# Kernel tuning notes

Hardware: AMD Instinct MI355X
Metric: run time of the kernel (lower is better)

The kernel has to match this reference:

```python
import jax, jax.numpy as jnp
import numpy as np

M, IN, OUT, K = 16384, 1024, 1024, 12


def setup_inputs() -> dict:
    key = jax.random.key(0)
    ks = jax.random.split(key, 7)
    x = jax.random.normal(ks[0], (M, IN), dtype=jnp.float32)
    # grid: per-feature linspace(-2,2) plus noise so the per-row sort is nontrivial
    base = jnp.linspace(-2.0, 2.0, K, dtype=jnp.float32)
    grid = jnp.broadcast_to(base, (IN, K)) + 0.3 * jax.random.normal(ks[1], (IN, K), dtype=jnp.float32)
    coeffs = 0.1 * jax.random.normal(ks[2], (IN, K), dtype=jnp.float32)
    knot_alive = 3.0 * jnp.ones((IN, K), dtype=jnp.float32) + 0.5 * jax.random.normal(ks[3], (IN, K), dtype=jnp.float32)
    proj_w = jax.random.normal(ks[4], (OUT, IN), dtype=jnp.float32) / np.sqrt(IN)
    proj_b = jax.random.normal(ks[5], (OUT,), dtype=jnp.float32) * 0.01
    res_w = jax.random.normal(ks[6], (OUT, IN), dtype=jnp.float32) / np.sqrt(IN)
    return {"x": x, "grid": grid, "coeffs": coeffs, "knot_alive": knot_alive,
            "proj_w": proj_w, "proj_b": proj_b, "res_w": res_w}


def _eval_adaptive_spline(x, grid, coeffs, knot_alive):
    # x: (M, in)  grid/coeffs/knot_alive: (in, K)
    K_ = grid.shape[1]
    sort_idx = jnp.argsort(grid, axis=1)
    sorted_grid = jnp.take_along_axis(grid, sort_idx, axis=1)
    sorted_coeffs = jnp.take_along_axis(coeffs, sort_idx, axis=1)
    sorted_alive = jnp.take_along_axis(knot_alive, sort_idx, axis=1)
    masked_coeffs = sorted_coeffs * jax.nn.sigmoid(sorted_alive)  # (in, K)

    grid_min = sorted_grid[:, 0]   # (in,)
    grid_max = sorted_grid[:, -1]  # (in,)
    x_clamped = jnp.minimum(jnp.maximum(x, grid_min[None, :]), grid_max[None, :])
    grid_range = jnp.maximum(grid_max - grid_min, 1e-6)
    x_norm = (x_clamped - grid_min[None, :]) / grid_range[None, :] * (K_ - 1)  # (M, in)
    idx_l = jnp.clip(x_norm.astype(jnp.int32), 0, K_ - 2)  # trunc == floor (x_norm >= 0)
    frac = x_norm - idx_l.astype(x.dtype)

    feat = jnp.arange(x.shape[1])[None, :]  # (1, in)
    c_left = masked_coeffs[feat, idx_l]      # (M, in)
    c_right = masked_coeffs[feat, idx_l + 1]  # (M, in)
    return c_left + frac * (c_right - c_left)


def reference(x, grid, coeffs, knot_alive, proj_w, proj_b, res_w):
    spline_out = _eval_adaptive_spline(x, grid, coeffs, knot_alive)  # (M, in)
    return spline_out @ proj_w.T + proj_b + x @ res_w.T  # (M, out)
```

## Files before the change

kernel.cpp:

```cpp
#include <hip/hip_runtime.h>
#include <hip/hip_bf16.h>

typedef unsigned short u16;
typedef float f32x4 __attribute__((ext_vector_type(4)));
typedef __bf16 bf16x8 __attribute__((ext_vector_type(8)));
typedef u16 u16x8 __attribute__((ext_vector_type(8)));

#define M_DIM 16384
#define IN_DIM 1024
#define OUT_DIM 1024
#define K_KNOTS 12
#define KCAT 2048


__device__ __forceinline__ u16 f2bf(float f) {
    unsigned int u = __builtin_bit_cast(unsigned int, f);
    u = u + 0x7FFFu + ((u >> 16) & 1u);
    return (u16)(u >> 16);
}

__device__ __forceinline__ void gload_lds16(const void* g, void* l) {
    __builtin_amdgcn_global_load_lds(
        (const __attribute__((address_space(1))) unsigned int*)g,
        (__attribute__((address_space(3))) unsigned int*)l, 16, 0, 0);
}

__global__ void prep_kernel(const float* __restrict__ grid,
                            const float* __restrict__ coeffs,
                            const float* __restrict__ alive,
                            float* __restrict__ pmc,
                            float* __restrict__ pgmin,
                            float* __restrict__ pscale)
{
    int i = blockIdx.x * blockDim.x + threadIdx.x;
    if (i >= IN_DIM) return;
    float g[K_KNOTS], c[K_KNOTS], a[K_KNOTS];
    for (int k = 0; k < K_KNOTS; ++k) {
        g[k] = grid[i * K_KNOTS + k];
        c[k] = coeffs[i * K_KNOTS + k];
        a[k] = alive[i * K_KNOTS + k];
    }
    for (int k = 1; k < K_KNOTS; ++k) {
        float gk = g[k], ck = c[k], ak = a[k];
        int j = k - 1;
        while (j >= 0 && g[j] > gk) {
            g[j + 1] = g[j]; c[j + 1] = c[j]; a[j + 1] = a[j]; --j;
        }
        g[j + 1] = gk; c[j + 1] = ck; a[j + 1] = ak;
    }
    for (int k = 0; k < K_KNOTS; ++k)
        pmc[i * K_KNOTS + k] = c[k] / (1.0f + expf(-a[k]));
    pgmin[i] = g[0];
    pscale[i] = (float)(K_KNOTS - 1) / fmaxf(g[K_KNOTS - 1] - g[0], 1e-6f);
}

__global__ __launch_bounds__(256) void conv_w_kernel(
    const float* __restrict__ pw, const float* __restrict__ rw,
    u16* __restrict__ Bw)
{
    const int n16 = blockIdx.x;
    const int tid = threadIdx.x;
    #pragma unroll 1
    for (int j = 0; j < 16; ++j) {
        int s = j * 256 + tid;
        int kc = s >> 6, l = s & 63;
        int row = n16 * 16 + (l & 15);
        int k = kc * 32 + ((l >> 4) & 3) * 8;
        const float* src = (k < IN_DIM) ? &pw[(long)row * IN_DIM + k]
                                        : &rw[(long)row * IN_DIM + (k - IN_DIM)];
        float4 v0 = *(const float4*)src;
        float4 v1 = *(const float4*)(src + 4);
        u16x8 ov;
        ov[0] = f2bf(v0.x); ov[1] = f2bf(v0.y); ov[2] = f2bf(v0.z); ov[3] = f2bf(v0.w);
        ov[4] = f2bf(v1.x); ov[5] = f2bf(v1.y); ov[6] = f2bf(v1.z); ov[7] = f2bf(v1.w);
        *(u16x8*)&Bw[((long)n16 * 64 + kc) * 512 + l * 8] = ov;
    }
}

#define XT_STR 260

__global__ __launch_bounds__(256) void build_a_kernel(
    const float* __restrict__ x,
    const float* __restrict__ pmc,
    const float* __restrict__ pgmin,
    const float* __restrict__ pscale,
    u16* __restrict__ Abf)
{
    __shared__ float s_mc[IN_DIM * K_KNOTS];
    __shared__ float s_gmin[IN_DIM];
    __shared__ float s_scale[IN_DIM];
    __shared__ float xt[16 * XT_STR];
    const int tid = threadIdx.x;
    for (int i = tid; i < IN_DIM * K_KNOTS; i += 256) s_mc[i] = pmc[i];
    for (int i = tid; i < IN_DIM; i += 256) { s_gmin[i] = pgmin[i]; s_scale[i] = pscale[i]; }

    const int m16 = blockIdx.x;

    #pragma unroll 1
    for (int c0 = 0; c0 < IN_DIM; c0 += 256) {
        __syncthreads();

        #pragma unroll
        for (int p = 0; p < 4; ++p) {
            int idx = p * 256 + tid;
            int r = idx >> 6, lc = (idx & 63) * 4;
            float4 v = *(const float4*)&x[(long)(m16 * 16 + r) * IN_DIM + c0 + lc];
            *(float4*)&xt[r * XT_STR + lc] = v;
        }
        __syncthreads();

        #pragma unroll
        for (int p = 0; p < 2; ++p) {
            int s = p * 256 + tid;
            int kc_l = s >> 6, l = s & 63;
            int r = l & 15;
            int cb = kc_l * 32 + ((l >> 4) & 3) * 8;
            const float* xp = &xt[r * XT_STR + cb];
            float4 v0 = *(const float4*)xp;
            float4 v1 = *(const float4*)(xp + 4);
            float xs[8] = {v0.x, v0.y, v0.z, v0.w, v1.x, v1.y, v1.z, v1.w};
            u16x8 so, co;
            #pragma unroll
            for (int e = 0; e < 8; ++e) {
                int i = c0 + cb + e;
                float xx = xs[e];
                float xn = (xx - s_gmin[i]) * s_scale[i];
                xn = fminf(fmaxf(xn, 0.0f), (float)(K_KNOTS - 1));
                int li = (int)xn;
                if (li > K_KNOTS - 2) li = K_KNOTS - 2;
                float frac = xn - (float)li;
                float cl = s_mc[i * K_KNOTS + li];
                float cr = s_mc[i * K_KNOTS + li + 1];
                so[e] = f2bf(cl + frac * (cr - cl));
                co[e] = f2bf(xx);
            }
            long kcS = (long)m16 * 64 + (c0 >> 5) + kc_l;
            *(u16x8*)&Abf[kcS * 512 + l * 8] = so;
            *(u16x8*)&Abf[(kcS + 32) * 512 + l * 8] = co;
        }
    }
}

#define TBK 64
#define NT (KCAT / TBK)
#define MSTR 32768L

#define BAR()     asm volatile("s_barrier" ::: "memory")
#define VM6BAR()  asm volatile("s_waitcnt vmcnt(6)\ns_barrier" ::: "memory")
#define LGKM0()   do { asm volatile("s_waitcnt lgkmcnt(0)" ::: "memory"); \
                       __builtin_amdgcn_sched_barrier(0); } while (0)

#define READ_A(buf, kk, mh) \
    _Pragma("unroll") \
    for (int m_ = 0; m_ < 4; ++m_) \
        af[m_] = *(const bf16x8*)&lds[(buf) + (kk)*8192 + (wm*8 + (mh)*4 + m_)*512 + loff];

#define READ_B(buf, kk) \
    _Pragma("unroll") \
    for (int n_ = 0; n_ < 4; ++n_) \
        bfr[n_] = *(const bf16x8*)&lds[32768 + (buf) + (kk)*8192 + (wn*4 + n_)*512 + loff];

#define MFMA16(base) \
    __builtin_amdgcn_s_setprio(1); \
    _Pragma("unroll") \
    for (int m_ = 0; m_ < 4; ++m_) \
        _Pragma("unroll") \
        for (int n_ = 0; n_ < 4; ++n_) \
            acc[(base) + m_][n_] = __builtin_amdgcn_mfma_f32_16x16x32_bf16( \
                af[m_], bfr[n_], acc[(base) + m_][n_], 0, 0, 0); \
    __builtin_amdgcn_s_setprio(0);

#define STAGE_A(Tidx, kk, buf) do { \
    gload_lds16(pAf +          ((long)((Tidx)*2 + (kk))) * 512, &lds[(buf) + (kk)*8192 + d0]); \
    gload_lds16(pAf + 8*MSTR + ((long)((Tidx)*2 + (kk))) * 512, &lds[(buf) + (kk)*8192 + d1]); } while (0)
#define STAGE_B(Tidx, kk, buf) do { \
    gload_lds16(pBf +          ((long)((Tidx)*2 + (kk))) * 512, &lds[32768 + (buf) + (kk)*8192 + d0]); \
    gload_lds16(pBf + 8*MSTR + ((long)((Tidx)*2 + (kk))) * 512, &lds[32768 + (buf) + (kk)*8192 + d1]); } while (0)

__global__ __launch_bounds__(512, 2) void gemm_kernel(
    const u16* __restrict__ A,
    const u16* __restrict__ B,
    const float* __restrict__ bias,
    float* __restrict__ C)
{
    __shared__ __align__(16) u16 lds[65536];

    const int tid  = threadIdx.x;
    const int lane = tid & 63;
    const int wave = tid >> 6;
    const int wm   = wave >> 2;
    const int wn   = wave & 3;

    int wgid = (blockIdx.x & 7) * 32 + (blockIdx.x >> 3);
    const int brow = (wgid >> 2) * 256;
    const int bcol = (wgid & 3) * 256;

    const u16* pAf = A + ((long)(brow >> 4) + wave) * MSTR + lane * 8;
    const u16* pBf = B + ((long)(bcol >> 4) + wave) * MSTR + lane * 8;

    const int d0 = tid * 8;
    const int d1 = 4096 + tid * 8;
    const int loff = lane * 8;

    f32x4 acc[8][4] = {};
    bf16x8 af[4], bfr[4];

    STAGE_A(0, 0, 0);
    STAGE_B(0, 0, 0);
    STAGE_A(0, 1, 0);
    STAGE_B(0, 1, 0);
    STAGE_B(1, 0, 16384);
    STAGE_A(1, 0, 16384);
    STAGE_B(1, 1, 16384);
    VM6BAR();

    #pragma unroll 1
    for (int t = 0; t < NT / 2; ++t) {
        const int T  = 2 * t;
        const int T1 = T + 1;
        const int T2 = (T + 2 < NT) ? T + 2 : 0;
        const int T3 = (T + 3 < NT) ? T + 3 : 0;

        READ_A(0, 0, 0); READ_B(0, 0);
        STAGE_A(T1, 1, 16384);
        BAR(); LGKM0();
        MFMA16(0);
        BAR();

        READ_A(0, 0, 1);
        STAGE_B(T2, 0, 0);
        BAR(); LGKM0();
        MFMA16(4);
        BAR();

        READ_A(0, 1, 0); READ_B(0, 1);
        STAGE_A(T2, 0, 0);
        BAR(); LGKM0();
        MFMA16(0);
        BAR();

        READ_A(0, 1, 1);
        STAGE_B(T2, 1, 0);
        VM6BAR(); LGKM0();
        MFMA16(4);
        BAR();

        READ_A(16384, 0, 0); READ_B(16384, 0);
        STAGE_A(T2, 1, 0);
        BAR(); LGKM0();
        MFMA16(0);
        BAR();

        READ_A(16384, 0, 1);
        STAGE_B(T3, 0, 16384);
        BAR(); LGKM0();
        MFMA16(4);
        BAR();

        READ_A(16384, 1, 0); READ_B(16384, 1);
        STAGE_A(T3, 0, 16384);
        BAR(); LGKM0();
        MFMA16(0);
        BAR();

        READ_A(16384, 1, 1);
        STAGE_B(T3, 1, 16384);
        VM6BAR(); LGKM0();
        MFMA16(4);
        BAR();
    }

    const int crow0 = brow + wm * 128 + (lane >> 4) * 4;
    const int ccol0 = bcol + wn * 64 + (lane & 15);
    float bv[4];
    #pragma unroll
    for (int n = 0; n < 4; ++n) bv[n] = bias[ccol0 + n * 16];
    #pragma unroll
    for (int m = 0; m < 8; ++m) {
        #pragma unroll
        for (int n = 0; n < 4; ++n) {
            #pragma unroll
            for (int j = 0; j < 4; ++j) {
                int row = crow0 + m * 16 + j;
                C[(long)row * OUT_DIM + ccol0 + n * 16] = acc[m][n][j] + bv[n];
            }
        }
    }
}

extern "C" void kernel_launch(void* const* d_in, const int* in_sizes, int n_in,
                              void* d_out, int out_size, void* d_ws, size_t ws_size,
                              hipStream_t stream) {
    const float* x      = (const float*)d_in[0];
    const float* grid   = (const float*)d_in[1];
    const float* coeffs = (const float*)d_in[2];
    const float* alive  = (const float*)d_in[3];
    const float* proj_w = (const float*)d_in[4];
    const float* proj_b = (const float*)d_in[5];
    const float* res_w  = (const float*)d_in[6];
    float* out = (float*)d_out;

    char* w = (char*)d_ws;
    size_t a_bytes = (size_t)M_DIM * KCAT * sizeof(u16);
    size_t b_bytes = (size_t)OUT_DIM * KCAT * sizeof(u16);
    u16* Abf   = (u16*)w;
    u16* Bw    = (u16*)(w + a_bytes);
    float* pmc = (float*)(w + a_bytes + b_bytes);
    float* pgmin  = pmc + IN_DIM * K_KNOTS;
    float* pscale = pgmin + IN_DIM;

    prep_kernel<<<(IN_DIM + 255) / 256, 256, 0, stream>>>(grid, coeffs, alive,
                                                          pmc, pgmin, pscale);
    conv_w_kernel<<<OUT_DIM / 16, 256, 0, stream>>>(proj_w, res_w, Bw);
    build_a_kernel<<<M_DIM / 16, 256, 0, stream>>>(x, pmc, pgmin, pscale, Abf);
    gemm_kernel<<<(M_DIM / 256) * (OUT_DIM / 256), 512, 0, stream>>>(Abf, Bw, proj_b, out);
}
```

Measured before the change: 114.7 us.

## Shrink GEMM tile to 128x256 with simple double buffer; batch spline rows

The GEMM kernel drops from a 256x256 tile with a deeply unrolled 8-phase LDS pipeline to a 128x256 tile with K-step 32. It uses a simple two-buffer loop and a smaller LDS footprint, with launch bounds raised to allow four blocks per CU. The A-building kernel now uses 512 threads and processes four 16-row groups per block, which amortises the per-block load of the spline tables into shared memory. The smaller GEMM tile lowers arithmetic intensity per block and the simpler loop leaves less overlap, traded for higher occupancy.

```diff
diff --git a/kernel.cpp b/kernel.cpp
--- a/kernel.cpp
+++ b/kernel.cpp
@@ -79,7 +79,7 @@
 
 #define XT_STR 260
 
-__global__ __launch_bounds__(256) void build_a_kernel(
+__global__ __launch_bounds__(512) void build_a_kernel(
     const float* __restrict__ x,
     const float* __restrict__ pmc,
     const float* __restrict__ pgmin,
@@ -91,99 +91,77 @@
     __shared__ float s_scale[IN_DIM];
     __shared__ float xt[16 * XT_STR];
     const int tid = threadIdx.x;
-    for (int i = tid; i < IN_DIM * K_KNOTS; i += 256) s_mc[i] = pmc[i];
-    for (int i = tid; i < IN_DIM; i += 256) { s_gmin[i] = pgmin[i]; s_scale[i] = pscale[i]; }
-
-    const int m16 = blockIdx.x;
+    for (int i = tid; i < IN_DIM * K_KNOTS; i += 512) s_mc[i] = pmc[i];
+    for (int i = tid; i < IN_DIM; i += 512) { s_gmin[i] = pgmin[i]; s_scale[i] = pscale[i]; }
 
     #pragma unroll 1
-    for (int c0 = 0; c0 < IN_DIM; c0 += 256) {
-        __syncthreads();
-
-        #pragma unroll
-        for (int p = 0; p < 4; ++p) {
-            int idx = p * 256 + tid;
-            int r = idx >> 6, lc = (idx & 63) * 4;
-            float4 v = *(const float4*)&x[(long)(m16 * 16 + r) * IN_DIM + c0 + lc];
-            *(float4*)&xt[r * XT_STR + lc] = v;
+    for (int g = 0; g < 4; ++g) {
+        const int m16 = blockIdx.x * 4 + g;
+        #pragma unroll 1
+        for (int c0 = 0; c0 < IN_DIM; c0 += 256) {
+            __syncthreads();
+
+            #pragma unroll
+            for (int p = 0; p < 2; ++p) {
+                int idx = p * 512 + tid;
+                int r = idx >> 6, lc = (idx & 63) * 4;
+                float4 v = *(const float4*)&x[(long)(m16 * 16 + r) * IN_DIM + c0 + lc];
+                *(float4*)&xt[r * XT_STR + lc] = v;
+            }
+            __syncthreads();
+
+            {
+                int kc_l = tid >> 6, l = tid & 63;
+                int r = l & 15;
+                int cb = kc_l * 32 + ((l >> 4) & 3) * 8;
+                const float* xp = &xt[r * XT_STR + cb];
+                float4 v0 = *(const float4*)xp;
+                float4 v1 = *(const float4*)(xp + 4);
+                float xs[8] = {v0.x, v0.y, v0.z, v0.w, v1.x, v1.y, v1.z, v1.w};
+                u16x8 so, co;
+                #pragma unroll
+                for (int e = 0; e < 8; ++e) {
+                    int i = c0 + cb + e;
+                    float xx = xs[e];
+                    float xn = (xx - s_gmin[i]) * s_scale[i];
+                    xn = fminf(fmaxf(xn, 0.0f), (float)(K_KNOTS - 1));
+                    int li = (int)xn;
+                    if (li > K_KNOTS - 2) li = K_KNOTS - 2;
+                    float frac = xn - (float)li;
+                    float cl = s_mc[i * K_KNOTS + li];
+                    float cr = s_mc[i * K_KNOTS + li + 1];
+                    so[e] = f2bf(cl + frac * (cr - cl));
+                    co[e] = f2bf(xx);
+                }
+                long kcS = (long)m16 * 64 + (c0 >> 5) + kc_l;
+                *(u16x8*)&Abf[kcS * 512 + l * 8] = so;
+                *(u16x8*)&Abf[(kcS + 32) * 512 + l * 8] = co;
+            }
         }
-        __syncthreads();
-
-        #pragma unroll
-        for (int p = 0; p < 2; ++p) {
-            int s = p * 256 + tid;
-            int kc_l = s >> 6, l = s & 63;
-            int r = l & 15;
-            int cb = kc_l * 32 + ((l >> 4) & 3) * 8;
-            const float* xp = &xt[r * XT_STR + cb];
-            float4 v0 = *(const float4*)xp;
-            float4 v1 = *(const float4*)(xp + 4);
-            float xs[8] = {v0.x, v0.y, v0.z, v0.w, v1.x, v1.y, v1.z, v1.w};
-            u16x8 so, co;
-            #pragma unroll
-            for (int e = 0; e < 8; ++e) {
-                int i = c0 + cb + e;
-                float xx = xs[e];
-                float xn = (xx - s_gmin[i]) * s_scale[i];
-                xn = fminf(fmaxf(xn, 0.0f), (float)(K_KNOTS - 1));
-                int li = (int)xn;
-                if (li > K_KNOTS - 2) li = K_KNOTS - 2;
-                float frac = xn - (float)li;
-                float cl = s_mc[i * K_KNOTS + li];
-                float cr = s_mc[i * K_KNOTS + li + 1];
-                so[e] = f2bf(cl + frac * (cr - cl));
-                co[e] = f2bf(xx);
-            }
-            long kcS = (long)m16 * 64 + (c0 >> 5) + kc_l;
-            *(u16x8*)&Abf[kcS * 512 + l * 8] = so;
-            *(u16x8*)&Abf[(kcS + 32) * 512 + l * 8] = co;
-        }
-    }
-}
-
-#define TBK 64
+    }
+}
+
+#define TBK 32
 #define NT (KCAT / TBK)
 #define MSTR 32768L
 
 #define BAR()     asm volatile("s_barrier" ::: "memory")
-#define VM6BAR()  asm volatile("s_waitcnt vmcnt(6)\ns_barrier" ::: "memory")
+#define VM3BAR()  asm volatile("s_waitcnt vmcnt(3)\ns_barrier" ::: "memory")
 #define LGKM0()   do { asm volatile("s_waitcnt lgkmcnt(0)" ::: "memory"); \
                        __builtin_amdgcn_sched_barrier(0); } while (0)
 
-#define READ_A(buf, kk, mh) \
-    _Pragma("unroll") \
-    for (int m_ = 0; m_ < 4; ++m_) \
-        af[m_] = *(const bf16x8*)&lds[(buf) + (kk)*8192 + (wm*8 + (mh)*4 + m_)*512 + loff];
-
-#define READ_B(buf, kk) \
-    _Pragma("unroll") \
-    for (int n_ = 0; n_ < 4; ++n_) \
-        bfr[n_] = *(const bf16x8*)&lds[32768 + (buf) + (kk)*8192 + (wn*4 + n_)*512 + loff];
-
-#define MFMA16(base) \
-    __builtin_amdgcn_s_setprio(1); \
-    _Pragma("unroll") \
-    for (int m_ = 0; m_ < 4; ++m_) \
-        _Pragma("unroll") \
-        for (int n_ = 0; n_ < 4; ++n_) \
-            acc[(base) + m_][n_] = __builtin_amdgcn_mfma_f32_16x16x32_bf16( \
-                af[m_], bfr[n_], acc[(base) + m_][n_], 0, 0, 0); \
-    __builtin_amdgcn_s_setprio(0);
-
-#define STAGE_A(Tidx, kk, buf) do { \
-    gload_lds16(pAf +          ((long)((Tidx)*2 + (kk))) * 512, &lds[(buf) + (kk)*8192 + d0]); \
-    gload_lds16(pAf + 8*MSTR + ((long)((Tidx)*2 + (kk))) * 512, &lds[(buf) + (kk)*8192 + d1]); } while (0)
-#define STAGE_B(Tidx, kk, buf) do { \
-    gload_lds16(pBf +          ((long)((Tidx)*2 + (kk))) * 512, &lds[32768 + (buf) + (kk)*8192 + d0]); \
-    gload_lds16(pBf + 8*MSTR + ((long)((Tidx)*2 + (kk))) * 512, &lds[32768 + (buf) + (kk)*8192 + d1]); } while (0)
-
-__global__ __launch_bounds__(512, 2) void gemm_kernel(
+#define STAGE2(T, cb) do { \
+    gload_lds16(pAf +          ((long)(T)) * 512, &lds[(cb) * 4096 + tid * 8]); \
+    gload_lds16(pBf +          ((long)(T)) * 512, &lds[8192 + (cb) * 8192 + tid * 8]); \
+    gload_lds16(pBf + 8*MSTR + ((long)(T)) * 512, &lds[8192 + (cb) * 8192 + 4096 + tid * 8]); } while (0)
+
+__global__ __launch_bounds__(512, 4) void gemm_kernel(
     const u16* __restrict__ A,
     const u16* __restrict__ B,
     const float* __restrict__ bias,
     float* __restrict__ C)
 {
-    __shared__ __align__(16) u16 lds[65536];
+    __shared__ __align__(16) u16 lds[24576];
 
     const int tid  = threadIdx.x;
     const int lane = tid & 63;
@@ -191,92 +169,57 @@
     const int wm   = wave >> 2;
     const int wn   = wave & 3;
 
-    int wgid = (blockIdx.x & 7) * 32 + (blockIdx.x >> 3);
-    const int brow = (wgid >> 2) * 256;
+    int wgid = (blockIdx.x & 7) * 64 + (blockIdx.x >> 3);
+    const int brow = (wgid >> 2) * 128;
     const int bcol = (wgid & 3) * 256;
 
     const u16* pAf = A + ((long)(brow >> 4) + wave) * MSTR + lane * 8;
     const u16* pBf = B + ((long)(bcol >> 4) + wave) * MSTR + lane * 8;
 
-    const int d0 = tid * 8;
-    const int d1 = 4096 + tid * 8;
     const int loff = lane * 8;
 
-    f32x4 acc[8][4] = {};
+    f32x4 acc[4][4] = {};
     bf16x8 af[4], bfr[4];
 
-    STAGE_A(0, 0, 0);
-    STAGE_B(0, 0, 0);
-    STAGE_A(0, 1, 0);
-    STAGE_B(0, 1, 0);
-    STAGE_B(1, 0, 16384);
-    STAGE_A(1, 0, 16384);
-    STAGE_B(1, 1, 16384);
-    VM6BAR();
+    STAGE2(0, 0);
+    STAGE2(1, 1);
+    VM3BAR();
 
     #pragma unroll 1
-    for (int t = 0; t < NT / 2; ++t) {
-        const int T  = 2 * t;
-        const int T1 = T + 1;
-        const int T2 = (T + 2 < NT) ? T + 2 : 0;
-        const int T3 = (T + 3 < NT) ? T + 3 : 0;
-
-        READ_A(0, 0, 0); READ_B(0, 0);
-        STAGE_A(T1, 1, 16384);
-        BAR(); LGKM0();
-        MFMA16(0);
+    for (int t = 0; t < NT; ++t) {
+        const int cb = t & 1;
+        const int ab = cb * 4096;
+        const int bb = 8192 + cb * 8192;
+
+        #pragma unroll
+        for (int m_ = 0; m_ < 4; ++m_)
+            af[m_] = *(const bf16x8*)&lds[ab + (wm * 4 + m_) * 512 + loff];
+        #pragma unroll
+        for (int n_ = 0; n_ < 4; ++n_)
+            bfr[n_] = *(const bf16x8*)&lds[bb + (wn * 4 + n_) * 512 + loff];
+        LGKM0();
+        __builtin_amdgcn_s_setprio(1);
+        #pragma unroll
+        for (int m_ = 0; m_ < 4; ++m_)
+            #pragma unroll
+            for (int n_ = 0; n_ < 4; ++n_)
+                acc[m_][n_] = __builtin_amdgcn_mfma_f32_16x16x32_bf16(
+                    af[m_], bfr[n_], acc[m_][n_], 0, 0, 0);
+        __builtin_amdgcn_s_setprio(0);
         BAR();
 
-        READ_A(0, 0, 1);
-        STAGE_B(T2, 0, 0);
-        BAR(); LGKM0();
-        MFMA16(4);
-        BAR();
-
-        READ_A(0, 1, 0); READ_B(0, 1);
-        STAGE_A(T2, 0, 0);
-        BAR(); LGKM0();
-        MFMA16(0);
-        BAR();
-
-        READ_A(0, 1, 1);
-        STAGE_B(T2, 1, 0);
-        VM6BAR(); LGKM0();
-        MFMA16(4);
-        BAR();
-
-        READ_A(16384, 0, 0); READ_B(16384, 0);
-        STAGE_A(T2, 1, 0);
-        BAR(); LGKM0();
-        MFMA16(0);
-        BAR();
-
-        READ_A(16384, 0, 1);
-        STAGE_B(T3, 0, 16384);
-        BAR(); LGKM0();
-        MFMA16(4);
-        BAR();
-
-        READ_A(16384, 1, 0); READ_B(16384, 1);
-        STAGE_A(T3, 0, 16384);
-        BAR(); LGKM0();
-        MFMA16(0);
-        BAR();
-
-        READ_A(16384, 1, 1);
-        STAGE_B(T3, 1, 16384);
-        VM6BAR(); LGKM0();
-        MFMA16(4);
-        BAR();
-    }
-
-    const int crow0 = brow + wm * 128 + (lane >> 4) * 4;
+        const int T2 = (t + 2) & 63;
+        STAGE2(T2, cb);
+        VM3BAR();
+    }
+
+    const int crow0 = brow + wm * 64 + (lane >> 4) * 4;
     const int ccol0 = bcol + wn * 64 + (lane & 15);
     float bv[4];
     #pragma unroll
     for (int n = 0; n < 4; ++n) bv[n] = bias[ccol0 + n * 16];
     #pragma unroll
-    for (int m = 0; m < 8; ++m) {
+    for (int m = 0; m < 4; ++m) {
         #pragma unroll
         for (int n = 0; n < 4; ++n) {
             #pragma unroll
@@ -312,6 +255,6 @@
     prep_kernel<<<(IN_DIM + 255) / 256, 256, 0, stream>>>(grid, coeffs, alive,
                                                           pmc, pgmin, pscale);
     conv_w_kernel<<<OUT_DIM / 16, 256, 0, stream>>>(proj_w, res_w, Bw);
-    build_a_kernel<<<M_DIM / 16, 256, 0, stream>>>(x, pmc, pgmin, pscale, Abf);
-    gemm_kernel<<<(M_DIM / 256) * (OUT_DIM / 256), 512, 0, stream>>>(Abf, Bw, proj_b, out);
-}
+    build_a_kernel<<<M_DIM / 64, 512, 0, stream>>>(x, pmc, pgmin, pscale, Abf);
+    gemm_kernel<<<(M_DIM / 128) * (OUT_DIM / 256), 512, 0, stream>>>(Abf, Bw, proj_b, out);
+}
```

Measured after the change: 108.4 us. 5.5% less time.
